# Performance work log

Hardware: AMD Instinct MI355X
Metric: run time of the kernel (lower is better)

Reference implementation:

```python
import jax, jax.numpy as jnp
import numpy as np

BATCH = 2048
FEAT = 512
HIDDEN = 512
NUM_CLASSES = 1000


def setup_inputs() -> dict:
    key = jax.random.key(0)
    k1, k2, k3, k4 = jax.random.split(key, 4)
    Z = jax.random.normal(k1, (BATCH, FEAT), dtype=jnp.float32)
    y = jax.random.randint(k2, (BATCH,), 0, NUM_CLASSES)
    W1 = jax.random.normal(k3, (NUM_CLASSES, HIDDEN, FEAT), dtype=jnp.float32)
    b1 = jnp.zeros((NUM_CLASSES, HIDDEN), dtype=jnp.float32)
    W2 = jax.random.normal(k4, (NUM_CLASSES, HIDDEN), dtype=jnp.float32)
    b2 = jnp.zeros((NUM_CLASSES,), dtype=jnp.float32)
    return {"Z": Z, "y": y, "W1": W1, "b1": b1, "W2": W2, "b2": b2}


def reference(Z, y, W1, b1, W2, b2):
    # Per-sample class-indexed weights: w1 [B, H, F], b1 [B, H], w2 [B, H], b2 [B]
    # hidden = tanh(w1 @ Z + b1); out = w2 . hidden + b2
    h = jnp.tanh(jnp.einsum('bhf,bf->bh', W1[y], Z) + b1[y])  # [B, H]
    op = jnp.einsum('bh,bh->b', W2[y], h) + b2[y]             # [B]
    return op
```

## Files before the change

kernel.cpp:

```cpp
#include <hip/hip_runtime.h>
#include <math.h>

#define BATCH 2048
#define FEAT 512
#define HIDDEN 512
#define NUM_CLASSES 1000
#define SCHUNK 8
#define NTHREADS 256
#define QROWS 128
#define NQ 4
#define MAXN 16
#define DSTRIDE 20

#define WS_TMPIDX (NUM_CLASSES * DSTRIDE)

__device__ __forceinline__ float fast_tanh(float x) {
    float e = __expf(2.0f * x);
    return 1.0f - 2.0f / (e + 1.0f);
}

__global__ __launch_bounds__(1024) void gather_kernel(const int* __restrict__ y,
                                                      int* __restrict__ ws,
                                                      float* __restrict__ out) {
    __shared__ int s_cnt[NUM_CLASSES];
    __shared__ int s_nact;
    const int tid = threadIdx.x;
    if (tid == 0) s_nact = 0;
    if (tid < NUM_CLASSES) s_cnt[tid] = 0;
    out[tid] = 0.0f;
    out[tid + 1024] = 0.0f;
    __syncthreads();
    #pragma unroll
    for (int i = 0; i < 2; ++i) {
        const int b = tid + i * 1024;
        const int cls = y[b];
        const int p = atomicAdd(&s_cnt[cls], 1);
        if (p < MAXN) ws[WS_TMPIDX + cls * MAXN + p] = b;
    }
    __syncthreads();
    if (tid < NUM_CLASSES) ws[tid * DSTRIDE] = -1;
    __syncthreads();
    if (tid < NUM_CLASSES) {
        const int cnt = s_cnt[tid];
        if (cnt > 0) {
            const int a = atomicAdd(&s_nact, 1);
            int* d = ws + a * DSTRIDE;
            d[0] = tid;
            d[1] = min(cnt, MAXN);
            #pragma unroll
            for (int k = 0; k < MAXN; ++k)
                d[4 + k] = (k < cnt) ? ws[WS_TMPIDX + tid * MAXN + k] : 0;
        }
    }
}

__global__ __launch_bounds__(NTHREADS) void disc2l_kernel(
    const float* __restrict__ Z, const int* __restrict__ ws,
    const float* __restrict__ W1, const float* __restrict__ b1,
    const float* __restrict__ W2, const float* __restrict__ b2,
    float* __restrict__ out)
{
    const int a       = blockIdx.x >> 2;
    const int quarter = blockIdx.x & 3;
    const int tid  = threadIdx.x;
    const int lane = tid & 63;
    const int wave = tid >> 6;
    const int q    = lane >> 4;
    const int ms   = lane & 15;

    const int* __restrict__ desc = ws + a * DSTRIDE;
    const int c = desc[0];
    if (c < 0) return;
    const int n = desc[1];

    __shared__ float s_z[SCHUNK][FEAT];
    __shared__ float s_b1[QROWS];
    __shared__ float s_w2[QROWS];
    __shared__ float s_part[4][SCHUNK];

    const int row0 = quarter * QROWS;
    const float* W1c = W1 + (size_t)c * HIDDEN * FEAT + (size_t)row0 * FEAT;

    float4 wa[8], wb[8];
    {
        const float4* Wa = (const float4*)(W1c + (size_t)(8 * wave + q) * FEAT);
        const float4* Wb = (const float4*)(W1c + (size_t)(8 * wave + 4 + q) * FEAT);
        #pragma unroll
        for (int k = 0; k < 8; ++k) { wa[k] = Wa[k * 16 + ms]; wb[k] = Wb[k * 16 + ms]; }
    }

    if (tid < 32)      ((float4*)s_b1)[tid]      = ((const float4*)(b1 + (size_t)c * HIDDEN + row0))[tid];
    else if (tid < 64) ((float4*)s_w2)[tid - 32] = ((const float4*)(W2 + (size_t)c * HIDDEN + row0))[tid - 32];

    const float b2c = (quarter == 0) ? b2[c] : 0.0f;

    for (int cb = 0; cb < n; cb += SCHUNK) {
        const int cn = min(SCHUNK, n - cb);

        if (cb > 0) {
            const float4* Wa = (const float4*)(W1c + (size_t)(8 * wave + q) * FEAT);
            const float4* Wb = (const float4*)(W1c + (size_t)(8 * wave + 4 + q) * FEAT);
            #pragma unroll
            for (int k = 0; k < 8; ++k) { wa[k] = Wa[k * 16 + ms]; wb[k] = Wb[k * 16 + ms]; }
        }

        #pragma unroll
        for (int s0 = 0; s0 < SCHUNK; s0 += 2) {
            const int s = s0 + (tid >> 7);
            if (s < cn) {
                const int zi = desc[4 + cb + s];
                ((float4*)s_z[s])[tid & 127] = ((const float4*)(Z + (size_t)zi * FEAT))[tid & 127];
            }
        }
        __syncthreads();

        float oacc = 0.0f;

        for (int g = wave; g < QROWS / 8; g += 4) {
            const int rla = 8 * g + q;
            const int rlb = 8 * g + 4 + q;

            float pa[SCHUNK], pb[SCHUNK];
            #pragma unroll
            for (int s = 0; s < SCHUNK; ++s) { pa[s] = 0.0f; pb[s] = 0.0f; }

            #pragma unroll
            for (int k = 0; k < 8; ++k) {
                #pragma unroll
                for (int s = 0; s < SCHUNK; ++s) {
                    if (s < cn) {
                        const float4 zv = ((const float4*)(&s_z[s][k * 64]))[ms];
                        pa[s] += wa[k].x * zv.x + wa[k].y * zv.y
                               + wa[k].z * zv.z + wa[k].w * zv.w;
                        pb[s] += wb[k].x * zv.x + wb[k].y * zv.y
                               + wb[k].z * zv.z + wb[k].w * zv.w;
                    }
                }
            }

            if (g + 4 < QROWS / 8) {
                const float4* Wa = (const float4*)(W1c + (size_t)(8 * (g + 4) + q) * FEAT);
                const float4* Wb = (const float4*)(W1c + (size_t)(8 * (g + 4) + 4 + q) * FEAT);
                #pragma unroll
                for (int k = 0; k < 8; ++k) { wa[k] = Wa[k * 16 + ms]; wb[k] = Wb[k * 16 + ms]; }
            }

            #pragma unroll
            for (int s = 0; s < SCHUNK; ++s) {
                if (s < cn) {
                    pa[s] += __shfl_xor(pa[s], 1, 64);
                    pa[s] += __shfl_xor(pa[s], 2, 64);
                    pa[s] += __shfl_xor(pa[s], 4, 64);
                    pa[s] += __shfl_xor(pa[s], 8, 64);
                    pb[s] += __shfl_xor(pb[s], 1, 64);
                    pb[s] += __shfl_xor(pb[s], 2, 64);
                    pb[s] += __shfl_xor(pb[s], 4, 64);
                    pb[s] += __shfl_xor(pb[s], 8, 64);
                }
            }

            if (ms < cn) {
                float va = pa[0], vb = pb[0];
                #pragma unroll
                for (int s = 1; s < SCHUNK; ++s)
                    if (ms == s) { va = pa[s]; vb = pb[s]; }
                const float ta = fast_tanh(va + s_b1[rla]);
                const float tb = fast_tanh(vb + s_b1[rlb]);
                oacc += s_w2[rla] * ta + s_w2[rlb] * tb;
            }
        }

        oacc += __shfl_xor(oacc, 16, 64);
        oacc += __shfl_xor(oacc, 32, 64);
        if (lane < cn) s_part[wave][lane] = oacc;
        __syncthreads();
        if (tid < cn) {
            float o = b2c;
            #pragma unroll
            for (int w = 0; w < 4; ++w) o += s_part[w][tid];
            atomicAdd(&out[desc[4 + cb + tid]], o);
        }
    }
}

extern "C" void kernel_launch(void* const* d_in, const int* in_sizes, int n_in,
                              void* d_out, int out_size, void* d_ws, size_t ws_size,
                              hipStream_t stream) {
    const float* Z  = (const float*)d_in[0];
    const int*   y  = (const int*)d_in[1];
    const float* W1 = (const float*)d_in[2];
    const float* b1 = (const float*)d_in[3];
    const float* W2 = (const float*)d_in[4];
    const float* b2 = (const float*)d_in[5];
    float* out = (float*)d_out;
    int*   ws  = (int*)d_ws;

    gather_kernel<<<1, 1024, 0, stream>>>(y, ws, out);
    disc2l_kernel<<<NUM_CLASSES * NQ, NTHREADS, 0, stream>>>(Z, ws, W1, b1, W2, b2, out);
}
```

Measured before the change: 185.7 us.

## Replace static grid with persistent blocks pulling work items from an atomic queue

The main kernel now launches a fixed 1024 persistent blocks. Each block repeatedly grabs a (class, quarter) work item from a global atomic counter, where before it launched one block per class-quarter and had blocks for absent classes exit early. This removes the launch and scheduling cost of empty blocks and balances uneven per-class sample counts. The cost is a global atomic plus two block barriers per item, and the weight prefetch no longer overlaps across block boundaries.

```diff
diff --git a/kernel.cpp b/kernel.cpp
--- a/kernel.cpp
+++ b/kernel.cpp
@@ -11,8 +11,12 @@
 #define NQ 4
 #define MAXN 16
 #define DSTRIDE 20
-
-#define WS_TMPIDX (NUM_CLASSES * DSTRIDE)
+#define NBLOCKS 1024
+
+#define WS_QUEUE  0
+#define WS_NITEMS 1
+#define WS_DESC   16
+#define WS_TMPIDX (WS_DESC + NUM_CLASSES * DSTRIDE)
 
 __device__ __forceinline__ float fast_tanh(float x) {
     float e = __expf(2.0f * x);
@@ -25,7 +29,7 @@
     __shared__ int s_cnt[NUM_CLASSES];
     __shared__ int s_nact;
     const int tid = threadIdx.x;
-    if (tid == 0) s_nact = 0;
+    if (tid == 0) { s_nact = 0; ws[WS_QUEUE] = 0; }
     if (tid < NUM_CLASSES) s_cnt[tid] = 0;
     out[tid] = 0.0f;
     out[tid + 1024] = 0.0f;
@@ -38,13 +42,11 @@
         if (p < MAXN) ws[WS_TMPIDX + cls * MAXN + p] = b;
     }
     __syncthreads();
-    if (tid < NUM_CLASSES) ws[tid * DSTRIDE] = -1;
-    __syncthreads();
     if (tid < NUM_CLASSES) {
         const int cnt = s_cnt[tid];
         if (cnt > 0) {
             const int a = atomicAdd(&s_nact, 1);
-            int* d = ws + a * DSTRIDE;
+            int* d = ws + WS_DESC + a * DSTRIDE;
             d[0] = tid;
             d[1] = min(cnt, MAXN);
             #pragma unroll
@@ -52,133 +54,145 @@
                 d[4 + k] = (k < cnt) ? ws[WS_TMPIDX + tid * MAXN + k] : 0;
         }
     }
+    __syncthreads();
+    if (tid == 0) ws[WS_NITEMS] = s_nact * NQ;
 }
 
 __global__ __launch_bounds__(NTHREADS) void disc2l_kernel(
-    const float* __restrict__ Z, const int* __restrict__ ws,
+    const float* __restrict__ Z, int* __restrict__ ws,
     const float* __restrict__ W1, const float* __restrict__ b1,
     const float* __restrict__ W2, const float* __restrict__ b2,
     float* __restrict__ out)
 {
-    const int a       = blockIdx.x >> 2;
-    const int quarter = blockIdx.x & 3;
     const int tid  = threadIdx.x;
     const int lane = tid & 63;
     const int wave = tid >> 6;
     const int q    = lane >> 4;
     const int ms   = lane & 15;
 
-    const int* __restrict__ desc = ws + a * DSTRIDE;
-    const int c = desc[0];
-    if (c < 0) return;
-    const int n = desc[1];
-
+    __shared__ int   s_item;
     __shared__ float s_z[SCHUNK][FEAT];
     __shared__ float s_b1[QROWS];
     __shared__ float s_w2[QROWS];
     __shared__ float s_part[4][SCHUNK];
 
-    const int row0 = quarter * QROWS;
-    const float* W1c = W1 + (size_t)c * HIDDEN * FEAT + (size_t)row0 * FEAT;
-
-    float4 wa[8], wb[8];
-    {
-        const float4* Wa = (const float4*)(W1c + (size_t)(8 * wave + q) * FEAT);
-        const float4* Wb = (const float4*)(W1c + (size_t)(8 * wave + 4 + q) * FEAT);
-        #pragma unroll
-        for (int k = 0; k < 8; ++k) { wa[k] = Wa[k * 16 + ms]; wb[k] = Wb[k * 16 + ms]; }
-    }
-
-    if (tid < 32)      ((float4*)s_b1)[tid]      = ((const float4*)(b1 + (size_t)c * HIDDEN + row0))[tid];
-    else if (tid < 64) ((float4*)s_w2)[tid - 32] = ((const float4*)(W2 + (size_t)c * HIDDEN + row0))[tid - 32];
-
-    const float b2c = (quarter == 0) ? b2[c] : 0.0f;
-
-    for (int cb = 0; cb < n; cb += SCHUNK) {
-        const int cn = min(SCHUNK, n - cb);
-
-        if (cb > 0) {
+    const int n_items = ws[WS_NITEMS];
+
+    for (;;) {
+        __syncthreads();
+        if (tid == 0) s_item = atomicAdd(&ws[WS_QUEUE], 1);
+        __syncthreads();
+        const int item = s_item;
+        if (item >= n_items) return;
+
+        const int a       = item >> 2;
+        const int quarter = item & 3;
+        const int* __restrict__ desc = ws + WS_DESC + a * DSTRIDE;
+        const int c = desc[0];
+        const int n = desc[1];
+
+        const int row0 = quarter * QROWS;
+        const float* W1c = W1 + (size_t)c * HIDDEN * FEAT + (size_t)row0 * FEAT;
+
+        float4 wa[8], wb[8];
+        {
             const float4* Wa = (const float4*)(W1c + (size_t)(8 * wave + q) * FEAT);
             const float4* Wb = (const float4*)(W1c + (size_t)(8 * wave + 4 + q) * FEAT);
             #pragma unroll
             for (int k = 0; k < 8; ++k) { wa[k] = Wa[k * 16 + ms]; wb[k] = Wb[k * 16 + ms]; }
         }
 
-        #pragma unroll
-        for (int s0 = 0; s0 < SCHUNK; s0 += 2) {
-            const int s = s0 + (tid >> 7);
-            if (s < cn) {
-                const int zi = desc[4 + cb + s];
-                ((float4*)s_z[s])[tid & 127] = ((const float4*)(Z + (size_t)zi * FEAT))[tid & 127];
-            }
-        }
-        __syncthreads();
-
-        float oacc = 0.0f;
-
-        for (int g = wave; g < QROWS / 8; g += 4) {
-            const int rla = 8 * g + q;
-            const int rlb = 8 * g + 4 + q;
-
-            float pa[SCHUNK], pb[SCHUNK];
+        if (tid < 32)      ((float4*)s_b1)[tid]      = ((const float4*)(b1 + (size_t)c * HIDDEN + row0))[tid];
+        else if (tid < 64) ((float4*)s_w2)[tid - 32] = ((const float4*)(W2 + (size_t)c * HIDDEN + row0))[tid - 32];
+
+        const float b2c = (quarter == 0) ? b2[c] : 0.0f;
+
+        for (int cb = 0; cb < n; cb += SCHUNK) {
+            const int cn = min(SCHUNK, n - cb);
+
+            if (cb > 0) {
+                const float4* Wa = (const float4*)(W1c + (size_t)(8 * wave + q) * FEAT);
+                const float4* Wb = (const float4*)(W1c + (size_t)(8 * wave + 4 + q) * FEAT);
+                #pragma unroll
+                for (int k = 0; k < 8; ++k) { wa[k] = Wa[k * 16 + ms]; wb[k] = Wb[k * 16 + ms]; }
+            }
+
             #pragma unroll
-            for (int s = 0; s < SCHUNK; ++s) { pa[s] = 0.0f; pb[s] = 0.0f; }
-
-            #pragma unroll
-            for (int k = 0; k < 8; ++k) {
+            for (int s0 = 0; s0 < SCHUNK; s0 += 2) {
+                const int s = s0 + (tid >> 7);
+                if (s < cn) {
+                    const int zi = desc[4 + cb + s];
+                    ((float4*)s_z[s])[tid & 127] = ((const float4*)(Z + (size_t)zi * FEAT))[tid & 127];
+                }
+            }
+            __syncthreads();
+
+            float oacc = 0.0f;
+
+            for (int g = wave; g < QROWS / 8; g += 4) {
+                const int rla = 8 * g + q;
+                const int rlb = 8 * g + 4 + q;
+
+                float pa[SCHUNK], pb[SCHUNK];
+                #pragma unroll
+                for (int s = 0; s < SCHUNK; ++s) { pa[s] = 0.0f; pb[s] = 0.0f; }
+
+                #pragma unroll
+                for (int k = 0; k < 8; ++k) {
+                    #pragma unroll
+                    for (int s = 0; s < SCHUNK; ++s) {
+                        if (s < cn) {
+                            const float4 zv = ((const float4*)(&s_z[s][k * 64]))[ms];
+                            pa[s] += wa[k].x * zv.x + wa[k].y * zv.y
+                                   + wa[k].z * zv.z + wa[k].w * zv.w;
+                            pb[s] += wb[k].x * zv.x + wb[k].y * zv.y
+                                   + wb[k].z * zv.z + wb[k].w * zv.w;
+                        }
+                    }
+                }
+
+                if (g + 4 < QROWS / 8) {
+                    const float4* Wa = (const float4*)(W1c + (size_t)(8 * (g + 4) + q) * FEAT);
+                    const float4* Wb = (const float4*)(W1c + (size_t)(8 * (g + 4) + 4 + q) * FEAT);
+                    #pragma unroll
+                    for (int k = 0; k < 8; ++k) { wa[k] = Wa[k * 16 + ms]; wb[k] = Wb[k * 16 + ms]; }
+                }
+
                 #pragma unroll
                 for (int s = 0; s < SCHUNK; ++s) {
                     if (s < cn) {
-                        const float4 zv = ((const float4*)(&s_z[s][k * 64]))[ms];
-                        pa[s] += wa[k].x * zv.x + wa[k].y * zv.y
-                               + wa[k].z * zv.z + wa[k].w * zv.w;
-                        pb[s] += wb[k].x * zv.x + wb[k].y * zv.y
-                               + wb[k].z * zv.z + wb[k].w * zv.w;
+                        pa[s] += __shfl_xor(pa[s], 1, 64);
+                        pa[s] += __shfl_xor(pa[s], 2, 64);
+                        pa[s] += __shfl_xor(pa[s], 4, 64);
+                        pa[s] += __shfl_xor(pa[s], 8, 64);
+                        pb[s] += __shfl_xor(pb[s], 1, 64);
+                        pb[s] += __shfl_xor(pb[s], 2, 64);
+                        pb[s] += __shfl_xor(pb[s], 4, 64);
+                        pb[s] += __shfl_xor(pb[s], 8, 64);
                     }
                 }
-            }
-
-            if (g + 4 < QROWS / 8) {
-                const float4* Wa = (const float4*)(W1c + (size_t)(8 * (g + 4) + q) * FEAT);
-                const float4* Wb = (const float4*)(W1c + (size_t)(8 * (g + 4) + 4 + q) * FEAT);
-                #pragma unroll
-                for (int k = 0; k < 8; ++k) { wa[k] = Wa[k * 16 + ms]; wb[k] = Wb[k * 16 + ms]; }
-            }
-
-            #pragma unroll
-            for (int s = 0; s < SCHUNK; ++s) {
-                if (s < cn) {
-                    pa[s] += __shfl_xor(pa[s], 1, 64);
-                    pa[s] += __shfl_xor(pa[s], 2, 64);
-                    pa[s] += __shfl_xor(pa[s], 4, 64);
-                    pa[s] += __shfl_xor(pa[s], 8, 64);
-                    pb[s] += __shfl_xor(pb[s], 1, 64);
-                    pb[s] += __shfl_xor(pb[s], 2, 64);
-                    pb[s] += __shfl_xor(pb[s], 4, 64);
-                    pb[s] += __shfl_xor(pb[s], 8, 64);
-                }
-            }
-
-            if (ms < cn) {
-                float va = pa[0], vb = pb[0];
-                #pragma unroll
-                for (int s = 1; s < SCHUNK; ++s)
-                    if (ms == s) { va = pa[s]; vb = pb[s]; }
-                const float ta = fast_tanh(va + s_b1[rla]);
-                const float tb = fast_tanh(vb + s_b1[rlb]);
-                oacc += s_w2[rla] * ta + s_w2[rlb] * tb;
-            }
-        }
-
-        oacc += __shfl_xor(oacc, 16, 64);
-        oacc += __shfl_xor(oacc, 32, 64);
-        if (lane < cn) s_part[wave][lane] = oacc;
-        __syncthreads();
-        if (tid < cn) {
-            float o = b2c;
-            #pragma unroll
-            for (int w = 0; w < 4; ++w) o += s_part[w][tid];
-            atomicAdd(&out[desc[4 + cb + tid]], o);
+
+                if (ms < cn) {
+                    float va = pa[0], vb = pb[0];
+                    #pragma unroll
+                    for (int s = 1; s < SCHUNK; ++s)
+                        if (ms == s) { va = pa[s]; vb = pb[s]; }
+                    const float ta = fast_tanh(va + s_b1[rla]);
+                    const float tb = fast_tanh(vb + s_b1[rlb]);
+                    oacc += s_w2[rla] * ta + s_w2[rlb] * tb;
+                }
+            }
+
+            oacc += __shfl_xor(oacc, 16, 64);
+            oacc += __shfl_xor(oacc, 32, 64);
+            if (lane < cn) s_part[wave][lane] = oacc;
+            __syncthreads();
+            if (tid < cn) {
+                float o = b2c;
+                #pragma unroll
+                for (int w = 0; w < 4; ++w) o += s_part[w][tid];
+                atomicAdd(&out[desc[4 + cb + tid]], o);
+            }
         }
     }
 }
@@ -196,5 +210,5 @@
     int*   ws  = (int*)d_ws;
 
     gather_kernel<<<1, 1024, 0, stream>>>(y, ws, out);
-    disc2l_kernel<<<NUM_CLASSES * NQ, NTHREADS, 0, stream>>>(Z, ws, W1, b1, W2, b2, out);
-}
+    disc2l_kernel<<<NBLOCKS, NTHREADS, 0, stream>>>(Z, ws, W1, b1, W2, b2, out);
+}
```

New measurement: 190.1 us. 2.4% more time.
